# Kernel tuning notes

Measured on AMD Instinct MI355X. Metric: run time of the kernel, lower is better.

Reference implementation:

```python
import jax, jax.numpy as jnp
import numpy as np


def _conv2d_same(x, w, b):
    # x: [B,H,W,Cin], w: [kh,kw,Cin,Cout] (Keras HWIO), b: [Cout]
    y = jax.lax.conv_general_dilated(
        x, w, window_strides=(1, 1), padding='SAME',
        dimension_numbers=('NHWC', 'HWIO', 'NHWC'))
    return y + b


def _bilateral_slice_apply(grid, guide, image):
    # HDRNet bilateral_slice_apply with has_offset=True.
    # grid:  [B, gh, gw, gd, (ci+1)*co]
    # guide: [B, H, W] in [0,1]
    # image: [B, H, W, ci]
    B, gh, gw, gd, nc = grid.shape
    _, H, W, ci = image.shape
    co = nc // (ci + 1)
    dt = grid.dtype

    # Continuous grid coordinates (HDRNet convention: pixel centers, -0.5 shift)
    gx = (jnp.arange(W, dtype=dt) + 0.5) * gw / W - 0.5          # [W]
    gy = (jnp.arange(H, dtype=dt) + 0.5) * gh / H - 0.5          # [H]
    gz = guide.astype(dt) * gd - 0.5                             # [B,H,W]

    fx = jnp.floor(gx)
    fy = jnp.floor(gy)
    fz = jnp.floor(gz)
    bidx = jnp.arange(B)[:, None, None]                          # [B,1,1]

    coeffs = jnp.zeros((B, H, W, nc), dtype=dt)
    for dz in (0, 1):
        zz = fz + dz
        wz = jnp.maximum(1.0 - jnp.abs(gz - zz), 0.0)            # [B,H,W]
        zi = jnp.clip(zz.astype(jnp.int32), 0, gd - 1)           # [B,H,W]
        for dy in (0, 1):
            yy = fy + dy
            wy = jnp.maximum(1.0 - jnp.abs(gy - yy), 0.0)        # [H]
            yi = jnp.clip(yy.astype(jnp.int32), 0, gh - 1)       # [H]
            for dx in (0, 1):
                xx = fx + dx
                wx = jnp.maximum(1.0 - jnp.abs(gx - xx), 0.0)    # [W]
                xi = jnp.clip(xx.astype(jnp.int32), 0, gw - 1)   # [W]
                corner = grid[bidx, yi[None, :, None], xi[None, None, :], zi]  # [B,H,W,nc]
                w = wz * wy[None, :, None] * wx[None, None, :]   # [B,H,W]
                coeffs = coeffs + corner * w[..., None]

    # Per-pixel affine transform: coeffs -> [B,H,W,co,ci+1]
    A = coeffs.reshape(B, H, W, co, ci + 1)
    return jnp.einsum('bhwoi,bhwi->bhwo', A[..., :ci], image) + A[..., ci]


def setup_inputs() -> dict:
    key = jax.random.key(0)
    k1, k2, k3, k4 = jax.random.split(key, 4)
    B, H, W = 4, 1024, 1024
    grid = jax.random.normal(k1, (B, 16, 16, 8, 12), dtype=jnp.float32)
    guide = jax.random.uniform(k2, (B, H, W), dtype=jnp.float32)
    image = jax.random.normal(k3, (B, H, W, 3), dtype=jnp.float32)
    conv_w = jax.random.normal(k4, (3, 3, 3, 3), dtype=jnp.float32) * 0.1
    conv_b = jnp.zeros((3,), dtype=jnp.float32)
    return {'grid': grid, 'guide': guide, 'image': image,
            'conv_w': conv_w, 'conv_b': conv_b}


def reference(grid, guide, image, conv_w, conv_b):
    x = _conv2d_same(image, conv_w, conv_b)
    return _bilateral_slice_apply(grid, guide, x)
```

## Files before the change

### kernel.cpp

```cpp
#include <hip/hip_runtime.h>

#define H_  1024
#define W_  1024
#define B_  4
#define GH  16
#define GW  16
#define GD  8
#define NC  12
#define CELLF (GD * NC)
#define YROWF (GW * CELLF)

#define TW 64
#define TH 8
#define LROWS (TH + 2)
#define LCOLS (TW + 2)

typedef _Float16 h2 __attribute__((ext_vector_type(2)));

__device__ __forceinline__ h2 u2h(unsigned int u) { return __builtin_bit_cast(h2, u); }

__global__ __launch_bounds__(256, 8)
void fused_conv_slice(const float* __restrict__ grid,
                      const float* __restrict__ guide,
                      const float* __restrict__ image,
                      const float* __restrict__ conv_w,
                      const float* __restrict__ conv_b,
                      float* __restrict__ out)
{
    __shared__ float4 s_img4[LROWS][LCOLS];
    __shared__ uint4 s_t128[TH][3 * GD];
    __shared__ uint2 s_t64[TH][3 * GD];

    const int tx  = threadIdx.x;
    const int tyq = threadIdx.y;
    const int bx  = blockIdx.x;
    const int by  = blockIdx.y;
    const int b   = blockIdx.z;
    const int x0 = bx * TW;
    const int y0 = by * TH;
    const int tid = tyq * 64 + tx;
    const int imgbase = b * (H_ * W_ * 3);

    auto stage_px = [&](int rr, int c) {
        int yy = y0 - 1 + rr;
        int xx = x0 - 1 + c;
        float4 v = make_float4(0.f, 0.f, 0.f, 0.f);
        if (yy >= 0 && yy < H_ && xx >= 0 && xx < W_) {
            const float* p = image + imgbase + (yy * W_ + xx) * 3;
            v.x = p[0]; v.y = p[1]; v.z = p[2];
        }
        s_img4[rr][c] = v;
    };
    #pragma unroll
    for (int rr0 = 0; rr0 < LROWS; rr0 += 4) {
        int rr = rr0 + tyq;
        if (rr < LROWS) {
            stage_px(rr, tx);
            if (tx < 2) stage_px(rr, TW + tx);
        }
    }

    int cells[3];
    cells[0] = max(bx - 1, 0);
    cells[1] = bx;
    cells[2] = min(bx + 1, GW - 1);
    const float* gB = grid + b * (GH * GW * GD * NC);
    {
        int rr = tid >> 5;
        int le = tid & 31;
        int y  = y0 + rr;
        float gyf = (y + 0.5f) * (1.0f / 64.0f) - 0.5f;
        float fyf = floorf(gyf);
        float tyw = gyf - fyf;
        int iy = (int)fyf;
        int yi0 = min(max(iy, 0), GH - 1);
        int yi1 = min(max(iy + 1, 0), GH - 1);
        float wy0 = 1.0f - tyw, wy1 = tyw;
        const float4* G0 = (const float4*)(gB + yi0 * YROWF);
        const float4* G1 = (const float4*)(gB + yi1 * YROWF);
        #pragma unroll
        for (int k = 0; k < 3; ++k) {
            int e = le + k * 32;
            if (e < 72) {
                int s  = (e >= 48) ? 2 : ((e >= 24) ? 1 : 0);
                int re = e - s * 24;
                int z  = re / 3;
                int c4 = re - z * 3;
                int off = cells[s] * 24 + re;
                float4 v0 = G0[off], v1 = G1[off];
                h2 p0, p1;
                p0.x = (_Float16)(wy0 * v0.x + wy1 * v1.x);
                p0.y = (_Float16)(wy0 * v0.y + wy1 * v1.y);
                p1.x = (_Float16)(wy0 * v0.z + wy1 * v1.z);
                p1.y = (_Float16)(wy0 * v0.w + wy1 * v1.w);
                uint2 u;
                u.x = __builtin_bit_cast(unsigned int, p0);
                u.y = __builtin_bit_cast(unsigned int, p1);
                int ci = s * GD + z;
                unsigned short* dst = (c4 == 2)
                    ? (unsigned short*)&s_t64[rr][ci]
                    : (unsigned short*)&s_t128[rr][ci] + c4 * 4;
                *(uint2*)dst = u;
            }
        }
    }

    const int x = x0 + tx;
    const int lr = tyq * 2;
    const int guidebase = b * (H_ * W_);
    float g2[2];
    #pragma unroll
    for (int j = 0; j < 2; ++j)
        g2[j] = guide[guidebase + (y0 + lr + j) * W_ + x];

    float wgt[81];
    #pragma unroll
    for (int i = 0; i < 81; ++i) wgt[i] = conv_w[i];
    float bias0 = conv_b[0], bias1 = conv_b[1], bias2 = conv_b[2];

    __syncthreads();

    float4 r0[3], r1[3], r2[3];
    float acc2r[2][3];

    auto loadrow = [&](int r, float4* d) {
        d[0] = s_img4[r][tx];
        d[1] = s_img4[r][tx + 1];
        d[2] = s_img4[r][tx + 2];
    };
    auto conv3 = [&](const float4* ra, const float4* rb, const float4* rc, float* acc) {
        acc[0] = bias0; acc[1] = bias1; acc[2] = bias2;
        const float4* rows[3] = {ra, rb, rc};
        #pragma unroll
        for (int kh = 0; kh < 3; ++kh)
            #pragma unroll
            for (int kw = 0; kw < 3; ++kw) {
                float4 v4 = rows[kh][kw];
                float v[3] = {v4.x, v4.y, v4.z};
                #pragma unroll
                for (int ci = 0; ci < 3; ++ci) {
                    int wb = ((kh * 3 + kw) * 3 + ci) * 3;
                    acc[0] += v[ci] * wgt[wb + 0];
                    acc[1] += v[ci] * wgt[wb + 1];
                    acc[2] += v[ci] * wgt[wb + 2];
                }
            }
    };

    loadrow(lr + 0, r0); loadrow(lr + 1, r1); loadrow(lr + 2, r2);
    conv3(r0, r1, r2, acc2r[0]);
    loadrow(lr + 3, r0);
    conv3(r1, r2, r0, acc2r[1]);

    float gxf = (x + 0.5f) * (1.0f / 64.0f) - 0.5f;
    float fxf = floorf(gxf);
    float txw = gxf - fxf;
    float wxa = 1.0f - txw, wxb = txw;
    int s0 = (int)fxf - (bx - 1);

    const int outbase = b * (H_ * W_ * 3);

    #pragma unroll
    for (int j = 0; j < 2; ++j) {
        int y = y0 + lr + j;
        const uint4* T128 = &s_t128[lr + j][0];
        const uint2* T64  = &s_t64[lr + j][0];

        float gzf = g2[j] * 8.0f - 0.5f;
        float fzf = floorf(gzf);
        float tz = gzf - fzf;
        int iz = (int)fzf;
        int zb = min(max(iz, 0), GD - 2);
        float wA = (iz < 0) ? 1.0f : ((iz > GD - 2) ? 0.0f : (1.0f - tz));
        float wB = 1.0f - wA;

        float m0 = wxa * wA, m1 = wxa * wB, m2 = wxb * wA, m3 = wxb * wB;
        h2 m0h = {(_Float16)m0, (_Float16)m0};
        h2 m1h = {(_Float16)m1, (_Float16)m1};
        h2 m2h = {(_Float16)m2, (_Float16)m2};
        h2 m3h = {(_Float16)m3, (_Float16)m3};

        int ci0 = s0 * GD + zb;
        uint4 Alo = T128[ci0];          uint2 Ahi = T64[ci0];
        uint4 Blo = T128[ci0 + 1];      uint2 Bhi = T64[ci0 + 1];
        uint4 Clo = T128[ci0 + GD];     uint2 Chi = T64[ci0 + GD];
        uint4 Dlo = T128[ci0 + GD + 1]; uint2 Dhi = T64[ci0 + GD + 1];

        h2 A[6]  = {u2h(Alo.x), u2h(Alo.y), u2h(Alo.z), u2h(Alo.w), u2h(Ahi.x), u2h(Ahi.y)};
        h2 Bv[6] = {u2h(Blo.x), u2h(Blo.y), u2h(Blo.z), u2h(Blo.w), u2h(Bhi.x), u2h(Bhi.y)};
        h2 Cv[6] = {u2h(Clo.x), u2h(Clo.y), u2h(Clo.z), u2h(Clo.w), u2h(Chi.x), u2h(Chi.y)};
        h2 Dv[6] = {u2h(Dlo.x), u2h(Dlo.y), u2h(Dlo.z), u2h(Dlo.w), u2h(Dhi.x), u2h(Dhi.y)};

        h2 c[6];
        #pragma unroll
        for (int k = 0; k < 6; ++k)
            c[k] = __builtin_elementwise_fma(A[k], m0h,
                   __builtin_elementwise_fma(Bv[k], m1h,
                   __builtin_elementwise_fma(Cv[k], m2h, Dv[k] * m3h)));

        float a0 = acc2r[j][0], a1 = acc2r[j][1], a2 = acc2r[j][2];
        h2 q01 = {(_Float16)a0, (_Float16)a1};
        h2 q21 = {(_Float16)a2, (_Float16)1.0f};

        int oidx = outbase + (y * W_ + x) * 3;
        #pragma unroll
        for (int o3 = 0; o3 < 3; ++o3) {
            float t = __builtin_amdgcn_fdot2(c[2 * o3 + 1], q21, 0.0f, false);
            out[oidx + o3] = __builtin_amdgcn_fdot2(c[2 * o3], q01, t, false);
        }
    }
}

extern "C" void kernel_launch(void* const* d_in, const int* in_sizes, int n_in,
                              void* d_out, int out_size, void* d_ws, size_t ws_size,
                              hipStream_t stream) {
    const float* grid   = (const float*)d_in[0];
    const float* guide  = (const float*)d_in[1];
    const float* image  = (const float*)d_in[2];
    const float* conv_w = (const float*)d_in[3];
    const float* conv_b = (const float*)d_in[4];
    float* out = (float*)d_out;

    dim3 block(64, 4, 1);
    dim3 grid_dim(W_ / TW, H_ / TH, B_);
    fused_conv_slice<<<grid_dim, block, 0, stream>>>(grid, guide, image, conv_w, conv_b, out);
}
```

Before: 135.3 us.

## Double tile height, transpose LDS image layout, and use packed FP32 FMAs for conv

```diff
diff --git a/kernel.cpp b/kernel.cpp
--- a/kernel.cpp
+++ b/kernel.cpp
@@ -11,15 +11,19 @@
 #define YROWF (GW * CELLF)
 
 #define TW 64
-#define TH 8
+#define TH 16
 #define LROWS (TH + 2)
 #define LCOLS (TW + 2)
+#define RSTR  19
+#define CSTR  (3 * RSTR)
 
 typedef _Float16 h2 __attribute__((ext_vector_type(2)));
+typedef float    f2 __attribute__((ext_vector_type(2)));
 
 __device__ __forceinline__ h2 u2h(unsigned int u) { return __builtin_bit_cast(h2, u); }
-
-__global__ __launch_bounds__(256, 8)
+__device__ __forceinline__ f2 ldp(const float* p) { f2 r; __builtin_memcpy(&r, p, sizeof(r)); return r; }
+
+__global__ __launch_bounds__(256, 6)
 void fused_conv_slice(const float* __restrict__ grid,
                       const float* __restrict__ guide,
                       const float* __restrict__ image,
@@ -27,91 +31,89 @@
                       const float* __restrict__ conv_b,
                       float* __restrict__ out)
 {
-    __shared__ float4 s_img4[LROWS][LCOLS];
+    __shared__ float s_imgT[LCOLS * CSTR];
     __shared__ uint4 s_t128[TH][3 * GD];
-    __shared__ uint2 s_t64[TH][3 * GD];
+    __shared__ uint2 s_t64 [TH][3 * GD];
 
     const int tx  = threadIdx.x;
     const int tyq = threadIdx.y;
+    const int tid = tyq * 64 + tx;
     const int bx  = blockIdx.x;
     const int by  = blockIdx.y;
     const int b   = blockIdx.z;
     const int x0 = bx * TW;
     const int y0 = by * TH;
-    const int tid = tyq * 64 + tx;
     const int imgbase = b * (H_ * W_ * 3);
 
-    auto stage_px = [&](int rr, int c) {
-        int yy = y0 - 1 + rr;
-        int xx = x0 - 1 + c;
-        float4 v = make_float4(0.f, 0.f, 0.f, 0.f);
-        if (yy >= 0 && yy < H_ && xx >= 0 && xx < W_) {
-            const float* p = image + imgbase + (yy * W_ + xx) * 3;
-            v.x = p[0]; v.y = p[1]; v.z = p[2];
-        }
-        s_img4[rr][c] = v;
-    };
-    #pragma unroll
-    for (int rr0 = 0; rr0 < LROWS; rr0 += 4) {
-        int rr = rr0 + tyq;
-        if (rr < LROWS) {
-            stage_px(rr, tx);
-            if (tx < 2) stage_px(rr, TW + tx);
-        }
-    }
-
-    int cells[3];
-    cells[0] = max(bx - 1, 0);
-    cells[1] = bx;
-    cells[2] = min(bx + 1, GW - 1);
+    #pragma unroll
+    for (int it = 0; it < 5; ++it) {
+        int p = tid + it * 256;
+        if (p < LROWS * LCOLS) {
+            int rr = p / LCOLS;
+            int c  = p - rr * LCOLS;
+            int yy = y0 - 1 + rr;
+            int xx = x0 - 1 + c;
+            float v0 = 0.f, v1 = 0.f, v2 = 0.f;
+            if ((unsigned)yy < (unsigned)H_ && (unsigned)xx < (unsigned)W_) {
+                const float* q = image + imgbase + (yy * W_ + xx) * 3;
+                v0 = q[0]; v1 = q[1]; v2 = q[2];
+            }
+            float* d = s_imgT + c * CSTR + rr;
+            d[0]        = v0;
+            d[RSTR]     = v1;
+            d[2 * RSTR] = v2;
+        }
+    }
+
     const float* gB = grid + b * (GH * GW * GD * NC);
-    {
-        int rr = tid >> 5;
-        int le = tid & 31;
-        int y  = y0 + rr;
-        float gyf = (y + 0.5f) * (1.0f / 64.0f) - 0.5f;
-        float fyf = floorf(gyf);
-        float tyw = gyf - fyf;
-        int iy = (int)fyf;
-        int yi0 = min(max(iy, 0), GH - 1);
-        int yi1 = min(max(iy + 1, 0), GH - 1);
-        float wy0 = 1.0f - tyw, wy1 = tyw;
-        const float4* G0 = (const float4*)(gB + yi0 * YROWF);
-        const float4* G1 = (const float4*)(gB + yi1 * YROWF);
-        #pragma unroll
-        for (int k = 0; k < 3; ++k) {
-            int e = le + k * 32;
-            if (e < 72) {
-                int s  = (e >= 48) ? 2 : ((e >= 24) ? 1 : 0);
-                int re = e - s * 24;
-                int z  = re / 3;
-                int c4 = re - z * 3;
-                int off = cells[s] * 24 + re;
-                float4 v0 = G0[off], v1 = G1[off];
-                h2 p0, p1;
-                p0.x = (_Float16)(wy0 * v0.x + wy1 * v1.x);
-                p0.y = (_Float16)(wy0 * v0.y + wy1 * v1.y);
-                p1.x = (_Float16)(wy0 * v0.z + wy1 * v1.z);
-                p1.y = (_Float16)(wy0 * v0.w + wy1 * v1.w);
-                uint2 u;
-                u.x = __builtin_bit_cast(unsigned int, p0);
-                u.y = __builtin_bit_cast(unsigned int, p1);
-                int ci = s * GD + z;
-                unsigned short* dst = (c4 == 2)
-                    ? (unsigned short*)&s_t64[rr][ci]
-                    : (unsigned short*)&s_t128[rr][ci] + c4 * 4;
-                *(uint2*)dst = u;
-            }
-        }
-    }
-
-    const int x = x0 + tx;
-    const int lr = tyq * 2;
+    #pragma unroll
+    for (int it = 0; it < 2; ++it) {
+        int cidx = tid + it * 256;
+        if (cidx < TH * 24) {
+            int rr  = cidx / 24;
+            int rem = cidx - rr * 24;
+            int s   = rem >> 3;
+            int z   = rem & 7;
+            float gyf = (y0 + rr + 0.5f) * (1.0f / 64.0f) - 0.5f;
+            float fyf = floorf(gyf);
+            float tyw = gyf - fyf;
+            int iy  = (int)fyf;
+            int yi0 = min(max(iy, 0), GH - 1);
+            int yi1 = min(max(iy + 1, 0), GH - 1);
+            float wy0 = 1.0f - tyw, wy1 = tyw;
+            int cellx = min(max(bx - 1 + s, 0), GW - 1);
+            const float4* G0 = (const float4*)(gB + yi0 * YROWF + cellx * CELLF + z * NC);
+            const float4* G1 = (const float4*)(gB + yi1 * YROWF + cellx * CELLF + z * NC);
+            float4 a0 = G0[0], a1 = G0[1], a2 = G0[2];
+            float4 c0 = G1[0], c1 = G1[1], c2 = G1[2];
+            h2 p0, p1, p2, p3, p4, p5;
+            p0.x = (_Float16)(wy0 * a0.x + wy1 * c0.x); p0.y = (_Float16)(wy0 * a0.y + wy1 * c0.y);
+            p1.x = (_Float16)(wy0 * a0.z + wy1 * c0.z); p1.y = (_Float16)(wy0 * a0.w + wy1 * c0.w);
+            p2.x = (_Float16)(wy0 * a1.x + wy1 * c1.x); p2.y = (_Float16)(wy0 * a1.y + wy1 * c1.y);
+            p3.x = (_Float16)(wy0 * a1.z + wy1 * c1.z); p3.y = (_Float16)(wy0 * a1.w + wy1 * c1.w);
+            p4.x = (_Float16)(wy0 * a2.x + wy1 * c2.x); p4.y = (_Float16)(wy0 * a2.y + wy1 * c2.y);
+            p5.x = (_Float16)(wy0 * a2.z + wy1 * c2.z); p5.y = (_Float16)(wy0 * a2.w + wy1 * c2.w);
+            int ci = s * GD + z;
+            uint4 lo;
+            lo.x = __builtin_bit_cast(unsigned int, p0);
+            lo.y = __builtin_bit_cast(unsigned int, p1);
+            lo.z = __builtin_bit_cast(unsigned int, p2);
+            lo.w = __builtin_bit_cast(unsigned int, p3);
+            uint2 hi;
+            hi.x = __builtin_bit_cast(unsigned int, p4);
+            hi.y = __builtin_bit_cast(unsigned int, p5);
+            s_t128[rr][ci] = lo;
+            s_t64 [rr][ci] = hi;
+        }
+    }
+
+    const int x  = x0 + tx;
+    const int lr = tyq * 4;
     const int guidebase = b * (H_ * W_);
-    float g2[2];
-    #pragma unroll
-    for (int j = 0; j < 2; ++j)
-        g2[j] = guide[guidebase + (y0 + lr + j) * W_ + x];
+    float g4[4];
+    #pragma unroll
+    for (int j = 0; j < 4; ++j)
+        g4[j] = guide[guidebase + (y0 + lr + j) * W_ + x];
 
     float wgt[81];
     #pragma unroll
@@ -120,37 +122,39 @@
 
     __syncthreads();
 
-    float4 r0[3], r1[3], r2[3];
-    float acc2r[2][3];
-
-    auto loadrow = [&](int r, float4* d) {
-        d[0] = s_img4[r][tx];
-        d[1] = s_img4[r][tx + 1];
-        d[2] = s_img4[r][tx + 2];
-    };
-    auto conv3 = [&](const float4* ra, const float4* rb, const float4* rc, float* acc) {
-        acc[0] = bias0; acc[1] = bias1; acc[2] = bias2;
-        const float4* rows[3] = {ra, rb, rc};
+    f2 acc[2][3];
+    #pragma unroll
+    for (int o = 0; o < 3; ++o) {
+        float bo = (o == 0) ? bias0 : (o == 1) ? bias1 : bias2;
+        acc[0][o] = (f2){bo, bo};
+        acc[1][o] = (f2){bo, bo};
+    }
+
+    const float* pb0 = s_imgT + tx * CSTR + lr;
+    #pragma unroll
+    for (int kw = 0; kw < 3; ++kw) {
         #pragma unroll
-        for (int kh = 0; kh < 3; ++kh)
+        for (int ci = 0; ci < 3; ++ci) {
+            const float* pb = pb0 + kw * CSTR + ci * RSTR;
+            f2 q0 = ldp(pb + 0);
+            f2 q1 = ldp(pb + 1);
+            f2 q2 = ldp(pb + 2);
+            f2 q3 = ldp(pb + 3);
+            f2 q4 = ldp(pb + 4);
             #pragma unroll
-            for (int kw = 0; kw < 3; ++kw) {
-                float4 v4 = rows[kh][kw];
-                float v[3] = {v4.x, v4.y, v4.z};
+            for (int kh = 0; kh < 3; ++kh) {
+                f2 vA = (kh == 0) ? q0 : (kh == 1) ? q1 : q2;
+                f2 vB = (kh == 0) ? q2 : (kh == 1) ? q3 : q4;
                 #pragma unroll
-                for (int ci = 0; ci < 3; ++ci) {
-                    int wb = ((kh * 3 + kw) * 3 + ci) * 3;
-                    acc[0] += v[ci] * wgt[wb + 0];
-                    acc[1] += v[ci] * wgt[wb + 1];
-                    acc[2] += v[ci] * wgt[wb + 2];
+                for (int o = 0; o < 3; ++o) {
+                    float w = wgt[((kh * 3 + kw) * 3 + ci) * 3 + o];
+                    f2 ws = (f2){w, w};
+                    acc[0][o] = __builtin_elementwise_fma(vA, ws, acc[0][o]);
+                    acc[1][o] = __builtin_elementwise_fma(vB, ws, acc[1][o]);
                 }
             }
-    };
-
-    loadrow(lr + 0, r0); loadrow(lr + 1, r1); loadrow(lr + 2, r2);
-    conv3(r0, r1, r2, acc2r[0]);
-    loadrow(lr + 3, r0);
-    conv3(r1, r2, r0, acc2r[1]);
+        }
+    }
 
     float gxf = (x + 0.5f) * (1.0f / 64.0f) - 0.5f;
     float fxf = floorf(gxf);
@@ -161,14 +165,14 @@
     const int outbase = b * (H_ * W_ * 3);
 
     #pragma unroll
-    for (int j = 0; j < 2; ++j) {
-        int y = y0 + lr + j;
-        const uint4* T128 = &s_t128[lr + j][0];
-        const uint2* T64  = &s_t64[lr + j][0];
-
-        float gzf = g2[j] * 8.0f - 0.5f;
+    for (int j = 0; j < 4; ++j) {
+        int R = lr + j;
+        const uint4* T128 = &s_t128[R][0];
+        const uint2* T64  = &s_t64 [R][0];
+
+        float gzf = g4[j] * 8.0f - 0.5f;
         float fzf = floorf(gzf);
-        float tz = gzf - fzf;
+        float tz  = gzf - fzf;
         int iz = (int)fzf;
         int zb = min(max(iz, 0), GD - 2);
         float wA = (iz < 0) ? 1.0f : ((iz > GD - 2) ? 0.0f : (1.0f - tz));
@@ -198,11 +202,13 @@
                    __builtin_elementwise_fma(Bv[k], m1h,
                    __builtin_elementwise_fma(Cv[k], m2h, Dv[k] * m3h)));
 
-        float a0 = acc2r[j][0], a1 = acc2r[j][1], a2 = acc2r[j][2];
+        float a0 = acc[j >> 1][0][j & 1];
+        float a1 = acc[j >> 1][1][j & 1];
+        float a2 = acc[j >> 1][2][j & 1];
         h2 q01 = {(_Float16)a0, (_Float16)a1};
         h2 q21 = {(_Float16)a2, (_Float16)1.0f};
 
-        int oidx = outbase + (y * W_ + x) * 3;
+        int oidx = outbase + ((y0 + R) * W_ + x) * 3;
         #pragma unroll
         for (int o3 = 0; o3 < 3; ++o3) {
             float t = __builtin_amdgcn_fdot2(c[2 * o3 + 1], q21, 0.0f, false);
```

New measurement: 129.5 us. 1.04x faster.

## Load conv halo directly from global memory instead of LDS staging

Applied to the files above, without the earlier changes.

```diff
diff --git a/kernel.cpp b/kernel.cpp
--- a/kernel.cpp
+++ b/kernel.cpp
@@ -12,12 +12,47 @@
 
 #define TW 64
 #define TH 8
-#define LROWS (TH + 2)
-#define LCOLS (TW + 2)
 
 typedef _Float16 h2 __attribute__((ext_vector_type(2)));
 
 __device__ __forceinline__ h2 u2h(unsigned int u) { return __builtin_bit_cast(h2, u); }
+
+template<bool G>
+__device__ __forceinline__ void load3g(const float* base, int yy, int xx, float* d) {
+    if constexpr (!G) {
+        __builtin_memcpy(d, base + (yy * W_ + xx) * 3, 12);
+    } else {
+        d[0] = 0.f; d[1] = 0.f; d[2] = 0.f;
+        if (((unsigned)yy < (unsigned)H_) && ((unsigned)xx < (unsigned)W_))
+            __builtin_memcpy(d, base + (yy * W_ + xx) * 3, 12);
+    }
+}
+
+template<bool G>
+__device__ __forceinline__ void loadrow9(const float* base, int ry, int x, float* d) {
+    load3g<G>(base, ry, x - 1, d + 0);
+    load3g<G>(base, ry, x,     d + 3);
+    load3g<G>(base, ry, x + 1, d + 6);
+}
+
+__device__ __forceinline__ void conv3r(const float* a, const float* b, const float* c,
+                                       float* acc, const float* wgt,
+                                       float bias0, float bias1, float bias2) {
+    acc[0] = bias0; acc[1] = bias1; acc[2] = bias2;
+    const float* rows[3] = {a, b, c};
+    #pragma unroll
+    for (int kh = 0; kh < 3; ++kh)
+        #pragma unroll
+        for (int kw = 0; kw < 3; ++kw)
+            #pragma unroll
+            for (int ci = 0; ci < 3; ++ci) {
+                float v = rows[kh][kw * 3 + ci];
+                const float* wb = wgt + ((kh * 3 + kw) * 3 + ci) * 3;
+                acc[0] += v * wb[0];
+                acc[1] += v * wb[1];
+                acc[2] += v * wb[2];
+            }
+}
 
 __global__ __launch_bounds__(256, 8)
 void fused_conv_slice(const float* __restrict__ grid,
@@ -27,7 +62,6 @@
                       const float* __restrict__ conv_b,
                       float* __restrict__ out)
 {
-    __shared__ float4 s_img4[LROWS][LCOLS];
     __shared__ uint4 s_t128[TH][3 * GD];
     __shared__ uint2 s_t64[TH][3 * GD];
 
@@ -39,26 +73,7 @@
     const int x0 = bx * TW;
     const int y0 = by * TH;
     const int tid = tyq * 64 + tx;
-    const int imgbase = b * (H_ * W_ * 3);
-
-    auto stage_px = [&](int rr, int c) {
-        int yy = y0 - 1 + rr;
-        int xx = x0 - 1 + c;
-        float4 v = make_float4(0.f, 0.f, 0.f, 0.f);
-        if (yy >= 0 && yy < H_ && xx >= 0 && xx < W_) {
-            const float* p = image + imgbase + (yy * W_ + xx) * 3;
-            v.x = p[0]; v.y = p[1]; v.z = p[2];
-        }
-        s_img4[rr][c] = v;
-    };
-    #pragma unroll
-    for (int rr0 = 0; rr0 < LROWS; rr0 += 4) {
-        int rr = rr0 + tyq;
-        if (rr < LROWS) {
-            stage_px(rr, tx);
-            if (tx < 2) stage_px(rr, TW + tx);
-        }
-    }
+    const float* ib = image + b * (H_ * W_ * 3);
 
     int cells[3];
     cells[0] = max(bx - 1, 0);
@@ -118,39 +133,26 @@
     for (int i = 0; i < 81; ++i) wgt[i] = conv_w[i];
     float bias0 = conv_b[0], bias1 = conv_b[1], bias2 = conv_b[2];
 
+    const int R0 = y0 + lr;
+    float ra[9], rb[9], rc[9], rd[9];
+    const bool edge = (bx == 0) | (bx == (W_ / TW - 1)) |
+                      (by == 0) | (by == (H_ / TH - 1));
+    if (!edge) {
+        loadrow9<false>(ib, R0 - 1, x, ra);
+        loadrow9<false>(ib, R0 + 0, x, rb);
+        loadrow9<false>(ib, R0 + 1, x, rc);
+        loadrow9<false>(ib, R0 + 2, x, rd);
+    } else {
+        loadrow9<true>(ib, R0 - 1, x, ra);
+        loadrow9<true>(ib, R0 + 0, x, rb);
+        loadrow9<true>(ib, R0 + 1, x, rc);
+        loadrow9<true>(ib, R0 + 2, x, rd);
+    }
+    float acc2r[2][3];
+    conv3r(ra, rb, rc, acc2r[0], wgt, bias0, bias1, bias2);
+    conv3r(rb, rc, rd, acc2r[1], wgt, bias0, bias1, bias2);
+
     __syncthreads();
-
-    float4 r0[3], r1[3], r2[3];
-    float acc2r[2][3];
-
-    auto loadrow = [&](int r, float4* d) {
-        d[0] = s_img4[r][tx];
-        d[1] = s_img4[r][tx + 1];
-        d[2] = s_img4[r][tx + 2];
-    };
-    auto conv3 = [&](const float4* ra, const float4* rb, const float4* rc, float* acc) {
-        acc[0] = bias0; acc[1] = bias1; acc[2] = bias2;
-        const float4* rows[3] = {ra, rb, rc};
-        #pragma unroll
-        for (int kh = 0; kh < 3; ++kh)
-            #pragma unroll
-            for (int kw = 0; kw < 3; ++kw) {
-                float4 v4 = rows[kh][kw];
-                float v[3] = {v4.x, v4.y, v4.z};
-                #pragma unroll
-                for (int ci = 0; ci < 3; ++ci) {
-                    int wb = ((kh * 3 + kw) * 3 + ci) * 3;
-                    acc[0] += v[ci] * wgt[wb + 0];
-                    acc[1] += v[ci] * wgt[wb + 1];
-                    acc[2] += v[ci] * wgt[wb + 2];
-                }
-            }
-    };
-
-    loadrow(lr + 0, r0); loadrow(lr + 1, r1); loadrow(lr + 2, r2);
-    conv3(r0, r1, r2, acc2r[0]);
-    loadrow(lr + 3, r0);
-    conv3(r1, r2, r0, acc2r[1]);
 
     float gxf = (x + 0.5f) * (1.0f / 64.0f) - 0.5f;
     float fxf = floorf(gxf);
```

Result: slower. 146.9 us (+8.6%).
